# Kernel tuning notes

Hardware: AMD Instinct MI355X
Metric: run time of the kernel (lower is better)

The kernel has to match this reference:

```python
import jax, jax.numpy as jnp
import numpy as np

B, T, D_MODEL, HEAD_SIZE = 4, 2048, 1024, 128


def setup_inputs() -> dict:
    key = jax.random.key(0)
    ks = jax.random.split(key, 7)
    s = 1.0 / np.sqrt(D_MODEL)
    return {
        "x": jax.random.normal(ks[0], (B, T, D_MODEL), dtype=jnp.float32),
        "Wq": jax.random.uniform(ks[1], (HEAD_SIZE, D_MODEL), jnp.float32, -s, s),
        "bq": jax.random.uniform(ks[2], (HEAD_SIZE,), jnp.float32, -s, s),
        "Wk": jax.random.uniform(ks[3], (HEAD_SIZE, D_MODEL), jnp.float32, -s, s),
        "bk": jax.random.uniform(ks[4], (HEAD_SIZE,), jnp.float32, -s, s),
        "Wv": jax.random.uniform(ks[5], (HEAD_SIZE, D_MODEL), jnp.float32, -s, s),
        "bv": jax.random.uniform(ks[6], (HEAD_SIZE,), jnp.float32, -s, s),
    }


def reference(x, Wq, bq, Wk, bk, Wv, bv):
    # context is None -> context = x (self-attention)
    # k from x, q from context(=x), v from context(=x)
    k = jnp.einsum("btd,hd->bth", x, Wk) + bk  # [B,T,H]
    q = jnp.einsum("btd,hd->bth", x, Wq) + bq  # [B,T,H]
    v = jnp.einsum("btd,hd->bth", x, Wv) + bv  # [B,T,H]
    scale = q.shape[-1] ** -0.5
    wei = jnp.einsum("bqh,bkh->bqk", q, k) * scale  # [B,T,T]
    # NOTE: source registers tril = torch.ones(...), so mask==0 is never
    # true and masked_fill is a no-op -> unmasked softmax (faithful).
    wei = jax.nn.softmax(wei, axis=-1)
    # dropout p=0.0 -> identity
    return jnp.einsum("bqk,bkh->bqh", wei, v)  # [B,T,H]
```

## Files before the change

### kernel.cpp

```cpp
#include <hip/hip_runtime.h>
#include <hip/hip_bf16.h>

typedef __hip_bfloat16 bf16;
typedef __attribute__((ext_vector_type(4))) float f32x4;
typedef __attribute__((ext_vector_type(8))) short s16x8;

#define TSEQ 2048
#define NB 4
#define HS 128
#define DM 1024

__device__ __forceinline__ ushort f2bf(float f) {
  bf16 h = __float2bfloat16(f);
  return *reinterpret_cast<ushort*>(&h);
}

__global__ __launch_bounds__(256) void cvt4(const float* __restrict__ src,
                                            ushort* __restrict__ dst, int n4) {
  int i = blockIdx.x * 256 + threadIdx.x;
  if (i >= n4) return;
  const float4 v = reinterpret_cast<const float4*>(src)[i];
  ushort4 o;
  o.x = f2bf(v.x); o.y = f2bf(v.y); o.z = f2bf(v.z); o.w = f2bf(v.w);
  reinterpret_cast<ushort4*>(dst)[i] = o;
}

__global__ __launch_bounds__(256) void qkv_gemm(
    const ushort* __restrict__ A, const ushort* __restrict__ Bw,
    const float* __restrict__ bq, const float* __restrict__ bk,
    const float* __restrict__ bv,
    ushort* __restrict__ Qb, ushort* __restrict__ Kb, ushort* __restrict__ Vt) {
  __shared__ __align__(16) ushort sA[128 * 64];
  __shared__ __align__(16) ushort sB[128 * 64];
  const int tid = threadIdx.x;
  const int lane = tid & 63;
  const int wv = tid >> 6;
  const int cl = lane & 15;
  const int g4 = lane >> 4;
  const int m0 = blockIdx.x * 128;
  const int nt = blockIdx.y;
  const int n0 = nt * 128;
  const int wr = (wv >> 1) * 64, wc = (wv & 1) * 64;

  f32x4 acc[4][4] = {};

  for (int k0 = 0; k0 < DM; k0 += 64) {
    for (int i = 0; i < 4; ++i) {
      int c = tid + i * 256;
      int row = c >> 3, g = c & 7;
      s16x8 va = *reinterpret_cast<const s16x8*>(A + (size_t)(m0 + row) * DM + k0 + g * 8);
      *reinterpret_cast<s16x8*>((char*)sA + row * 128 + ((g ^ (row & 7)) << 4)) = va;
      s16x8 vb = *reinterpret_cast<const s16x8*>(Bw + (size_t)(n0 + row) * DM + k0 + g * 8);
      *reinterpret_cast<s16x8*>((char*)sB + row * 128 + ((g ^ (row & 7)) << 4)) = vb;
    }
    __syncthreads();
    for (int kk = 0; kk < 2; ++kk) {
      s16x8 af[4], bfg[4];
      for (int m4 = 0; m4 < 4; ++m4) {
        int row = wr + m4 * 16 + cl;
        int g = kk * 4 + g4;
        af[m4] = *reinterpret_cast<const s16x8*>((const char*)sA + row * 128 + ((g ^ (row & 7)) << 4));
      }
      for (int n4 = 0; n4 < 4; ++n4) {
        int row = wc + n4 * 16 + cl;
        int g = kk * 4 + g4;
        bfg[n4] = *reinterpret_cast<const s16x8*>((const char*)sB + row * 128 + ((g ^ (row & 7)) << 4));
      }
      for (int m4 = 0; m4 < 4; ++m4)
        for (int n4 = 0; n4 < 4; ++n4)
          acc[m4][n4] = __builtin_amdgcn_mfma_f32_16x16x32_bf16(af[m4], bfg[n4], acc[m4][n4], 0, 0, 0);
    }
    __syncthreads();
  }

  const float scale = 0.08838834764831845f;
  for (int m4 = 0; m4 < 4; ++m4)
    for (int n4 = 0; n4 < 4; ++n4) {
      int n_loc = wc + n4 * 16 + cl;
      for (int r = 0; r < 4; ++r) {
        int m = m0 + wr + m4 * 16 + g4 * 4 + r;
        float v = acc[m4][n4][r];
        if (nt == 0) {
          v = (v + bq[n_loc]) * scale;
          Qb[(size_t)m * HS + n_loc] = f2bf(v);
        } else if (nt == 1) {
          v = v + bk[n_loc];
          Kb[(size_t)m * HS + n_loc] = f2bf(v);
        } else {
          v = v + bv[n_loc];
          int bb = m >> 11, t = m & 2047;
          Vt[((size_t)bb * HS + n_loc) * TSEQ + t] = f2bf(v);
        }
      }
    }
}

__global__ __launch_bounds__(256) void attn(const ushort* __restrict__ Qg,
                                            const ushort* __restrict__ Kg,
                                            const ushort* __restrict__ Vt,
                                            float* __restrict__ out) {
  __shared__ __align__(16) char smem[4 * 10240 + 1024];
  const int tid = threadIdx.x;
  const int lane = tid & 63;
  const int wv = tid >> 6;
  const int cl = lane & 15;
  const int g4 = lane >> 4;
  const int b = blockIdx.x >> 6;
  const int q0 = (blockIdx.x & 63) << 5;

  char* sKVb = smem + wv * 10240;
  char* sPb = smem + wv * 10240 + 8192;
  float* sml = (float*)(smem + 40960);
  float* sO = (float*)smem;

  s16x8 qf_[2][4];
  {
    const ushort* qbase = Qg + (size_t)(b * TSEQ + q0) * HS;
    for (int qf = 0; qf < 2; ++qf)
      for (int kk = 0; kk < 4; ++kk)
        qf_[qf][kk] = *reinterpret_cast<const s16x8*>(qbase + (qf * 16 + cl) * HS + kk * 32 + g4 * 8);
  }

  f32x4 o_[2][8] = {};
  float m_[2][4], l_[2][4];
  for (int qf = 0; qf < 2; ++qf)
    for (int r = 0; r < 4; ++r) { m_[qf][r] = -3.0e38f; l_[qf][r] = 0.f; }

  const int kvwave = wv * 512;
  for (int ti = 0; ti < 16; ++ti) {
    const int kv0 = kvwave + ti * 32;
    {
      const ushort* kb = Kg + (size_t)(b * TSEQ + kv0) * HS;
      for (int i = 0; i < 8; ++i) {
        int c = lane + i * 64;
        int row = c >> 4, g = c & 15;
        s16x8 v = *reinterpret_cast<const s16x8*>(kb + row * HS + g * 8);
        *reinterpret_cast<s16x8*>(sKVb + row * 256 + ((g ^ (row & 7)) << 4)) = v;
      }
    }
    f32x4 s_[2][2] = {};
    for (int kk = 0; kk < 4; ++kk)
      for (int kvf = 0; kvf < 2; ++kvf) {
        int row = kvf * 16 + cl;
        int g = kk * 4 + g4;
        s16x8 bfg = *reinterpret_cast<const s16x8*>(sKVb + row * 256 + ((g ^ (row & 7)) << 4));
        s_[0][kvf] = __builtin_amdgcn_mfma_f32_16x16x32_bf16(qf_[0][kk], bfg, s_[0][kvf], 0, 0, 0);
        s_[1][kvf] = __builtin_amdgcn_mfma_f32_16x16x32_bf16(qf_[1][kk], bfg, s_[1][kvf], 0, 0, 0);
      }
    {
      const ushort* vb = Vt + (size_t)b * HS * TSEQ + kv0;
      for (int i = 0; i < 8; ++i) {
        int c = lane + i * 64;
        int d = c >> 2, g = c & 3;
        s16x8 v = *reinterpret_cast<const s16x8*>(vb + (size_t)d * TSEQ + g * 8);
        *reinterpret_cast<s16x8*>(sKVb + d * 64 + ((g ^ ((d >> 1) & 3)) << 4)) = v;
      }
    }
    float alpha[2][4];
    for (int qf = 0; qf < 2; ++qf)
      for (int r = 0; r < 4; ++r) {
        float mx = fmaxf(s_[qf][0][r], s_[qf][1][r]);
        for (int msk = 1; msk < 16; msk <<= 1) mx = fmaxf(mx, __shfl_xor(mx, msk, 64));
        float mn = fmaxf(m_[qf][r], mx);
        float al = __expf(m_[qf][r] - mn);
        m_[qf][r] = mn;
        float p0 = __expf(s_[qf][0][r] - mn);
        float p1 = __expf(s_[qf][1][r] - mn);
        s_[qf][0][r] = p0; s_[qf][1][r] = p1;
        float rs = p0 + p1;
        for (int msk = 1; msk < 16; msk <<= 1) rs += __shfl_xor(rs, msk, 64);
        l_[qf][r] = l_[qf][r] * al + rs;
        alpha[qf][r] = al;
      }
    for (int qf = 0; qf < 2; ++qf)
      for (int df = 0; df < 8; ++df)
        for (int r = 0; r < 4; ++r) o_[qf][df][r] *= alpha[qf][r];
    for (int qf = 0; qf < 2; ++qf)
      for (int kvf = 0; kvf < 2; ++kvf)
        for (int r = 0; r < 4; ++r) {
          int q = qf * 16 + g4 * 4 + r;
          int kv = kvf * 16 + cl;
          *reinterpret_cast<ushort*>(sPb + q * 64 + (((kv >> 3) ^ ((q >> 1) & 3)) << 4) + (kv & 7) * 2) =
              f2bf(s_[qf][kvf][r]);
        }
    s16x8 af[2];
    for (int qf = 0; qf < 2; ++qf) {
      int q = qf * 16 + cl;
      af[qf] = *reinterpret_cast<const s16x8*>(sPb + q * 64 + ((g4 ^ ((q >> 1) & 3)) << 4));
    }
    for (int df = 0; df < 8; ++df) {
      int d = df * 16 + cl;
      s16x8 vf = *reinterpret_cast<const s16x8*>(sKVb + d * 64 + ((g4 ^ ((d >> 1) & 3)) << 4));
      o_[0][df] = __builtin_amdgcn_mfma_f32_16x16x32_bf16(af[0], vf, o_[0][df], 0, 0, 0);
      o_[1][df] = __builtin_amdgcn_mfma_f32_16x16x32_bf16(af[1], vf, o_[1][df], 0, 0, 0);
    }
  }

  if (cl == 0)
    for (int qf = 0; qf < 2; ++qf)
      for (int r = 0; r < 4; ++r) {
        int row = qf * 16 + g4 * 4 + r;
        sml[(wv * 32 + row) * 2 + 0] = m_[qf][r];
        sml[(wv * 32 + row) * 2 + 1] = l_[qf][r];
      }
  __syncthreads();
  float fac[2][4];
  for (int qf = 0; qf < 2; ++qf)
    for (int r = 0; r < 4; ++r) {
      int row = qf * 16 + g4 * 4 + r;
      float M = -3.0e38f;
      for (int w = 0; w < 4; ++w) M = fmaxf(M, sml[(w * 32 + row) * 2]);
      float L = 0.f;
      for (int w = 0; w < 4; ++w) L += sml[(w * 32 + row) * 2 + 1] * __expf(sml[(w * 32 + row) * 2] - M);
      fac[qf][r] = __expf(m_[qf][r] - M) / L;
    }
  for (int w = 0; w < 4; ++w) {
    if (wv == w) {
      for (int qf = 0; qf < 2; ++qf)
        for (int df = 0; df < 8; ++df)
          for (int r = 0; r < 4; ++r) {
            int q = qf * 16 + g4 * 4 + r;
            int d = df * 16 + cl;
            float val = o_[qf][df][r] * fac[qf][r];
            if (w == 0) sO[q * HS + d] = val;
            else        sO[q * HS + d] += val;
          }
    }
    __syncthreads();
  }
  float* op = out + (size_t)(b * TSEQ + q0) * HS;
  for (int i = tid; i < 32 * HS; i += 256) op[i] = sO[i];
}

extern "C" void kernel_launch(void* const* d_in, const int* in_sizes, int n_in,
                              void* d_out, int out_size, void* d_ws, size_t ws_size,
                              hipStream_t stream) {
  const float* x = (const float*)d_in[0];
  const float* Wq = (const float*)d_in[1];
  const float* bq = (const float*)d_in[2];
  const float* Wk = (const float*)d_in[3];
  const float* bk = (const float*)d_in[4];
  const float* Wv = (const float*)d_in[5];
  const float* bv = (const float*)d_in[6];
  float* out = (float*)d_out;

  char* ws = (char*)d_ws;
  ushort* xb = (ushort*)ws;
  ushort* wc = (ushort*)(ws + 16777216);
  ushort* Qb = (ushort*)(ws + 17563648);
  ushort* Kb = (ushort*)(ws + 19660800);
  ushort* Vt = (ushort*)(ws + 21757952);

  cvt4<<<8192, 256, 0, stream>>>(x, xb, 2097152);
  cvt4<<<128, 256, 0, stream>>>(Wq, wc, 32768);
  cvt4<<<128, 256, 0, stream>>>(Wk, wc + 131072, 32768);
  cvt4<<<128, 256, 0, stream>>>(Wv, wc + 262144, 32768);
  qkv_gemm<<<dim3(64, 3), 256, 0, stream>>>(xb, wc, bq, bk, bv, Qb, Kb, Vt);
  attn<<<256, 256, 0, stream>>>(Qb, Kb, Vt, out);
}
```

Baseline: 227.7 us.

## Retile QKV GEMM and attention for more blocks, fuse weight casts

The three weight-conversion launches are merged into one kernel. The QKV GEMM uses 64-row tiles, which doubles the grid to 384 blocks, and it writes the transposed V through an LDS staging buffer so the global stores are coalesced. Attention now uses 16-query blocks with 8 waves that split the KV range and has a swizzled block order. The cross-wave combine now uses LDS atomics. The aim is to raise occupancy and CU utilization on small grids, at the cost of less reuse per block and more combine overhead.

```diff
diff --git a/kernel.cpp b/kernel.cpp
--- a/kernel.cpp
+++ b/kernel.cpp
@@ -25,38 +25,57 @@
   reinterpret_cast<ushort4*>(dst)[i] = o;
 }
 
+__global__ __launch_bounds__(256) void cvtW(const float* __restrict__ Wq,
+                                            const float* __restrict__ Wk,
+                                            const float* __restrict__ Wv,
+                                            ushort* __restrict__ dst) {
+  int bid = blockIdx.x;
+  int seg = bid >> 7;
+  int i = (bid & 127) * 256 + threadIdx.x;
+  const float* src = seg == 0 ? Wq : (seg == 1 ? Wk : Wv);
+  const float4 v = reinterpret_cast<const float4*>(src)[i];
+  ushort4 o;
+  o.x = f2bf(v.x); o.y = f2bf(v.y); o.z = f2bf(v.z); o.w = f2bf(v.w);
+  reinterpret_cast<ushort4*>(dst + (size_t)seg * 131072)[i] = o;
+}
+
 __global__ __launch_bounds__(256) void qkv_gemm(
     const ushort* __restrict__ A, const ushort* __restrict__ Bw,
     const float* __restrict__ bq, const float* __restrict__ bk,
     const float* __restrict__ bv,
     ushort* __restrict__ Qb, ushort* __restrict__ Kb, ushort* __restrict__ Vt) {
-  __shared__ __align__(16) ushort sA[128 * 64];
-  __shared__ __align__(16) ushort sB[128 * 64];
+  __shared__ __align__(16) ushort smem[12288];
+  ushort* sA = smem;
+  ushort* sB = smem + 4096;
   const int tid = threadIdx.x;
   const int lane = tid & 63;
   const int wv = tid >> 6;
   const int cl = lane & 15;
   const int g4 = lane >> 4;
-  const int m0 = blockIdx.x * 128;
+  const int m0 = blockIdx.x * 64;
   const int nt = blockIdx.y;
   const int n0 = nt * 128;
-  const int wr = (wv >> 1) * 64, wc = (wv & 1) * 64;
-
-  f32x4 acc[4][4] = {};
+  const int wr = (wv >> 1) * 32, wc = (wv & 1) * 64;
+
+  f32x4 acc[2][4] = {};
 
   for (int k0 = 0; k0 < DM; k0 += 64) {
-    for (int i = 0; i < 4; ++i) {
+    for (int i = 0; i < 2; ++i) {
       int c = tid + i * 256;
       int row = c >> 3, g = c & 7;
       s16x8 va = *reinterpret_cast<const s16x8*>(A + (size_t)(m0 + row) * DM + k0 + g * 8);
       *reinterpret_cast<s16x8*>((char*)sA + row * 128 + ((g ^ (row & 7)) << 4)) = va;
+    }
+    for (int i = 0; i < 4; ++i) {
+      int c = tid + i * 256;
+      int row = c >> 3, g = c & 7;
       s16x8 vb = *reinterpret_cast<const s16x8*>(Bw + (size_t)(n0 + row) * DM + k0 + g * 8);
       *reinterpret_cast<s16x8*>((char*)sB + row * 128 + ((g ^ (row & 7)) << 4)) = vb;
     }
     __syncthreads();
     for (int kk = 0; kk < 2; ++kk) {
-      s16x8 af[4], bfg[4];
-      for (int m4 = 0; m4 < 4; ++m4) {
+      s16x8 af[2], bfg[4];
+      for (int m4 = 0; m4 < 2; ++m4) {
         int row = wr + m4 * 16 + cl;
         int g = kk * 4 + g4;
         af[m4] = *reinterpret_cast<const s16x8*>((const char*)sA + row * 128 + ((g ^ (row & 7)) << 4));
@@ -66,7 +85,7 @@
         int g = kk * 4 + g4;
         bfg[n4] = *reinterpret_cast<const s16x8*>((const char*)sB + row * 128 + ((g ^ (row & 7)) << 4));
       }
-      for (int m4 = 0; m4 < 4; ++m4)
+      for (int m4 = 0; m4 < 2; ++m4)
         for (int n4 = 0; n4 < 4; ++n4)
           acc[m4][n4] = __builtin_amdgcn_mfma_f32_16x16x32_bf16(af[m4], bfg[n4], acc[m4][n4], 0, 0, 0);
     }
@@ -74,60 +93,78 @@
   }
 
   const float scale = 0.08838834764831845f;
-  for (int m4 = 0; m4 < 4; ++m4)
-    for (int n4 = 0; n4 < 4; ++n4) {
-      int n_loc = wc + n4 * 16 + cl;
-      for (int r = 0; r < 4; ++r) {
-        int m = m0 + wr + m4 * 16 + g4 * 4 + r;
-        float v = acc[m4][n4][r];
-        if (nt == 0) {
-          v = (v + bq[n_loc]) * scale;
-          Qb[(size_t)m * HS + n_loc] = f2bf(v);
-        } else if (nt == 1) {
-          v = v + bk[n_loc];
-          Kb[(size_t)m * HS + n_loc] = f2bf(v);
-        } else {
-          v = v + bv[n_loc];
-          int bb = m >> 11, t = m & 2047;
-          Vt[((size_t)bb * HS + n_loc) * TSEQ + t] = f2bf(v);
+  if (nt < 2) {
+    for (int m4 = 0; m4 < 2; ++m4)
+      for (int n4 = 0; n4 < 4; ++n4) {
+        int n_loc = wc + n4 * 16 + cl;
+        for (int r = 0; r < 4; ++r) {
+          int m = m0 + wr + m4 * 16 + g4 * 4 + r;
+          float v = acc[m4][n4][r];
+          if (nt == 0) {
+            v = (v + bq[n_loc]) * scale;
+            Qb[(size_t)m * HS + n_loc] = f2bf(v);
+          } else {
+            v = v + bk[n_loc];
+            Kb[(size_t)m * HS + n_loc] = f2bf(v);
+          }
         }
       }
-    }
-}
-
-__global__ __launch_bounds__(256) void attn(const ushort* __restrict__ Qg,
-                                            const ushort* __restrict__ Kg,
-                                            const ushort* __restrict__ Vt,
-                                            float* __restrict__ out) {
-  __shared__ __align__(16) char smem[4 * 10240 + 1024];
+  } else {
+    ushort* sT = smem;
+    for (int m4 = 0; m4 < 2; ++m4)
+      for (int n4 = 0; n4 < 4; ++n4) {
+        int n_loc = wc + n4 * 16 + cl;
+        for (int r = 0; r < 4; ++r) {
+          int ml = wr + m4 * 16 + g4 * 4 + r;
+          sT[n_loc * 68 + ml] = f2bf(acc[m4][n4][r] + bv[n_loc]);
+        }
+      }
+    __syncthreads();
+    const int bb = m0 >> 11;
+    const int t0 = m0 & 2047;
+    int n = tid >> 1, mh = (tid & 1) * 32;
+    ushort* dst = Vt + ((size_t)bb * HS + n) * TSEQ + t0 + mh;
+    for (int j = 0; j < 4; ++j) {
+      s16x8 v = *reinterpret_cast<const s16x8*>(sT + n * 68 + mh + j * 8);
+      *reinterpret_cast<s16x8*>(dst + j * 8) = v;
+    }
+  }
+}
+
+#define WLDS 9216
+__global__ __launch_bounds__(512, 4) void attn(const ushort* __restrict__ Qg,
+                                               const ushort* __restrict__ Kg,
+                                               const ushort* __restrict__ Vt,
+                                               float* __restrict__ out) {
+  __shared__ __align__(16) char smem[8 * WLDS + 1024];
   const int tid = threadIdx.x;
   const int lane = tid & 63;
   const int wv = tid >> 6;
   const int cl = lane & 15;
   const int g4 = lane >> 4;
-  const int b = blockIdx.x >> 6;
-  const int q0 = (blockIdx.x & 63) << 5;
-
-  char* sKVb = smem + wv * 10240;
-  char* sPb = smem + wv * 10240 + 8192;
-  float* sml = (float*)(smem + 40960);
+  const int bid = blockIdx.x;
+  const int swz = (bid & 7) * 64 + (bid >> 3);
+  const int b = swz >> 7;
+  const int q0 = (swz & 127) << 4;
+
+  char* sKVb = smem + wv * WLDS;
+  char* sPb = smem + wv * WLDS + 8192;
+  float* sml = (float*)(smem + 8 * WLDS);
   float* sO = (float*)smem;
 
-  s16x8 qf_[2][4];
+  s16x8 qf_[4];
   {
-    const ushort* qbase = Qg + (size_t)(b * TSEQ + q0) * HS;
-    for (int qf = 0; qf < 2; ++qf)
-      for (int kk = 0; kk < 4; ++kk)
-        qf_[qf][kk] = *reinterpret_cast<const s16x8*>(qbase + (qf * 16 + cl) * HS + kk * 32 + g4 * 8);
-  }
-
-  f32x4 o_[2][8] = {};
-  float m_[2][4], l_[2][4];
-  for (int qf = 0; qf < 2; ++qf)
-    for (int r = 0; r < 4; ++r) { m_[qf][r] = -3.0e38f; l_[qf][r] = 0.f; }
-
-  const int kvwave = wv * 512;
-  for (int ti = 0; ti < 16; ++ti) {
+    const ushort* qbase = Qg + (size_t)(b * TSEQ + q0 + cl) * HS;
+    for (int kk = 0; kk < 4; ++kk)
+      qf_[kk] = *reinterpret_cast<const s16x8*>(qbase + kk * 32 + g4 * 8);
+  }
+
+  f32x4 o_[8] = {};
+  float m_[4], l_[4];
+  for (int r = 0; r < 4; ++r) { m_[r] = -3.0e38f; l_[r] = 0.f; }
+
+  const int kvwave = wv * 256;
+  for (int ti = 0; ti < 8; ++ti) {
     const int kv0 = kvwave + ti * 32;
     {
       const ushort* kb = Kg + (size_t)(b * TSEQ + kv0) * HS;
@@ -138,14 +175,13 @@
         *reinterpret_cast<s16x8*>(sKVb + row * 256 + ((g ^ (row & 7)) << 4)) = v;
       }
     }
-    f32x4 s_[2][2] = {};
+    f32x4 s_[2] = {};
     for (int kk = 0; kk < 4; ++kk)
       for (int kvf = 0; kvf < 2; ++kvf) {
         int row = kvf * 16 + cl;
         int g = kk * 4 + g4;
         s16x8 bfg = *reinterpret_cast<const s16x8*>(sKVb + row * 256 + ((g ^ (row & 7)) << 4));
-        s_[0][kvf] = __builtin_amdgcn_mfma_f32_16x16x32_bf16(qf_[0][kk], bfg, s_[0][kvf], 0, 0, 0);
-        s_[1][kvf] = __builtin_amdgcn_mfma_f32_16x16x32_bf16(qf_[1][kk], bfg, s_[1][kvf], 0, 0, 0);
+        s_[kvf] = __builtin_amdgcn_mfma_f32_16x16x32_bf16(qf_[kk], bfg, s_[kvf], 0, 0, 0);
       }
     {
       const ushort* vb = Vt + (size_t)b * HS * TSEQ + kv0;
@@ -156,80 +192,63 @@
         *reinterpret_cast<s16x8*>(sKVb + d * 64 + ((g ^ ((d >> 1) & 3)) << 4)) = v;
       }
     }
-    float alpha[2][4];
-    for (int qf = 0; qf < 2; ++qf)
+    for (int r = 0; r < 4; ++r) {
+      float mx = fmaxf(s_[0][r], s_[1][r]);
+      for (int msk = 1; msk < 16; msk <<= 1) mx = fmaxf(mx, __shfl_xor(mx, msk, 64));
+      float mn = fmaxf(m_[r], mx);
+      float al = __expf(m_[r] - mn);
+      m_[r] = mn;
+      float p0 = __expf(s_[0][r] - mn);
+      float p1 = __expf(s_[1][r] - mn);
+      s_[0][r] = p0; s_[1][r] = p1;
+      float rs = p0 + p1;
+      for (int msk = 1; msk < 16; msk <<= 1) rs += __shfl_xor(rs, msk, 64);
+      l_[r] = l_[r] * al + rs;
+      for (int df = 0; df < 8; ++df) o_[df][r] *= al;
+    }
+    for (int kvf = 0; kvf < 2; ++kvf)
       for (int r = 0; r < 4; ++r) {
-        float mx = fmaxf(s_[qf][0][r], s_[qf][1][r]);
-        for (int msk = 1; msk < 16; msk <<= 1) mx = fmaxf(mx, __shfl_xor(mx, msk, 64));
-        float mn = fmaxf(m_[qf][r], mx);
-        float al = __expf(m_[qf][r] - mn);
-        m_[qf][r] = mn;
-        float p0 = __expf(s_[qf][0][r] - mn);
-        float p1 = __expf(s_[qf][1][r] - mn);
-        s_[qf][0][r] = p0; s_[qf][1][r] = p1;
-        float rs = p0 + p1;
-        for (int msk = 1; msk < 16; msk <<= 1) rs += __shfl_xor(rs, msk, 64);
-        l_[qf][r] = l_[qf][r] * al + rs;
-        alpha[qf][r] = al;
-      }
-    for (int qf = 0; qf < 2; ++qf)
-      for (int df = 0; df < 8; ++df)
-        for (int r = 0; r < 4; ++r) o_[qf][df][r] *= alpha[qf][r];
-    for (int qf = 0; qf < 2; ++qf)
-      for (int kvf = 0; kvf < 2; ++kvf)
-        for (int r = 0; r < 4; ++r) {
-          int q = qf * 16 + g4 * 4 + r;
-          int kv = kvf * 16 + cl;
-          *reinterpret_cast<ushort*>(sPb + q * 64 + (((kv >> 3) ^ ((q >> 1) & 3)) << 4) + (kv & 7) * 2) =
-              f2bf(s_[qf][kvf][r]);
-        }
-    s16x8 af[2];
-    for (int qf = 0; qf < 2; ++qf) {
-      int q = qf * 16 + cl;
-      af[qf] = *reinterpret_cast<const s16x8*>(sPb + q * 64 + ((g4 ^ ((q >> 1) & 3)) << 4));
-    }
+        int q = g4 * 4 + r;
+        int kv = kvf * 16 + cl;
+        *reinterpret_cast<ushort*>(sPb + q * 64 + (((kv >> 3) ^ ((q >> 1) & 3)) << 4) + (kv & 7) * 2) =
+            f2bf(s_[kvf][r]);
+      }
+    s16x8 af = *reinterpret_cast<const s16x8*>(sPb + cl * 64 + ((g4 ^ ((cl >> 1) & 3)) << 4));
     for (int df = 0; df < 8; ++df) {
       int d = df * 16 + cl;
       s16x8 vf = *reinterpret_cast<const s16x8*>(sKVb + d * 64 + ((g4 ^ ((d >> 1) & 3)) << 4));
-      o_[0][df] = __builtin_amdgcn_mfma_f32_16x16x32_bf16(af[0], vf, o_[0][df], 0, 0, 0);
-      o_[1][df] = __builtin_amdgcn_mfma_f32_16x16x32_bf16(af[1], vf, o_[1][df], 0, 0, 0);
+      o_[df] = __builtin_amdgcn_mfma_f32_16x16x32_bf16(af, vf, o_[df], 0, 0, 0);
     }
   }
 
   if (cl == 0)
-    for (int qf = 0; qf < 2; ++qf)
-      for (int r = 0; r < 4; ++r) {
-        int row = qf * 16 + g4 * 4 + r;
-        sml[(wv * 32 + row) * 2 + 0] = m_[qf][r];
-        sml[(wv * 32 + row) * 2 + 1] = l_[qf][r];
-      }
-  __syncthreads();
-  float fac[2][4];
-  for (int qf = 0; qf < 2; ++qf)
     for (int r = 0; r < 4; ++r) {
-      int row = qf * 16 + g4 * 4 + r;
-      float M = -3.0e38f;
-      for (int w = 0; w < 4; ++w) M = fmaxf(M, sml[(w * 32 + row) * 2]);
-      float L = 0.f;
-      for (int w = 0; w < 4; ++w) L += sml[(w * 32 + row) * 2 + 1] * __expf(sml[(w * 32 + row) * 2] - M);
-      fac[qf][r] = __expf(m_[qf][r] - M) / L;
-    }
-  for (int w = 0; w < 4; ++w) {
-    if (wv == w) {
-      for (int qf = 0; qf < 2; ++qf)
-        for (int df = 0; df < 8; ++df)
-          for (int r = 0; r < 4; ++r) {
-            int q = qf * 16 + g4 * 4 + r;
-            int d = df * 16 + cl;
-            float val = o_[qf][df][r] * fac[qf][r];
-            if (w == 0) sO[q * HS + d] = val;
-            else        sO[q * HS + d] += val;
-          }
-    }
-    __syncthreads();
-  }
+      int row = g4 * 4 + r;
+      sml[(wv * 16 + row) * 2 + 0] = m_[r];
+      sml[(wv * 16 + row) * 2 + 1] = l_[r];
+    }
+  __syncthreads();
+  float fac[4];
+  for (int r = 0; r < 4; ++r) {
+    int row = g4 * 4 + r;
+    float M = -3.0e38f;
+    for (int w = 0; w < 8; ++w) M = fmaxf(M, sml[(w * 16 + row) * 2]);
+    float L = 0.f;
+    for (int w = 0; w < 8; ++w) L += sml[(w * 16 + row) * 2 + 1] * __expf(sml[(w * 16 + row) * 2] - M);
+    fac[r] = __expf(m_[r] - M) / L;
+  }
+  __syncthreads();
+  for (int i = tid; i < 16 * HS; i += 512) sO[i] = 0.f;
+  __syncthreads();
+  for (int df = 0; df < 8; ++df)
+    for (int r = 0; r < 4; ++r) {
+      int q = g4 * 4 + r;
+      int d = df * 16 + cl;
+      atomicAdd(&sO[q * HS + d], o_[df][r] * fac[r]);
+    }
+  __syncthreads();
   float* op = out + (size_t)(b * TSEQ + q0) * HS;
-  for (int i = tid; i < 32 * HS; i += 256) op[i] = sO[i];
+  reinterpret_cast<float4*>(op)[tid] = reinterpret_cast<const float4*>(sO)[tid];
 }
 
 extern "C" void kernel_launch(void* const* d_in, const int* in_sizes, int n_in,
@@ -252,9 +271,7 @@
   ushort* Vt = (ushort*)(ws + 21757952);
 
   cvt4<<<8192, 256, 0, stream>>>(x, xb, 2097152);
-  cvt4<<<128, 256, 0, stream>>>(Wq, wc, 32768);
-  cvt4<<<128, 256, 0, stream>>>(Wk, wc + 131072, 32768);
-  cvt4<<<128, 256, 0, stream>>>(Wv, wc + 262144, 32768);
-  qkv_gemm<<<dim3(64, 3), 256, 0, stream>>>(xb, wc, bq, bk, bv, Qb, Kb, Vt);
-  attn<<<256, 256, 0, stream>>>(Qb, Kb, Vt, out);
-}
+  cvtW<<<384, 256, 0, stream>>>(Wq, Wk, Wv, wc);
+  qkv_gemm<<<dim3(128, 3), 256, 0, stream>>>(xb, wc, bq, bk, bv, Qb, Kb, Vt);
+  attn<<<512, 512, 0, stream>>>(Qb, Kb, Vt, out);
+}
```

New measurement: 215.8 us. 1.06x faster.
